# Optimization experiments

Measured on AMD Instinct MI355X. Metric: run time of the kernel, lower is better.

## Reference

```python
import jax, jax.numpy as jnp
import numpy as np

D = 256
H = 16
HD = D // H
N_BIAS = 6
B, E = 8, 1024


def _layernorm(x, g, b, eps=1e-5):
    mu = jnp.mean(x, axis=-1, keepdims=True)
    var = jnp.mean(jnp.square(x - mu), axis=-1, keepdims=True)
    return (x - mu) * jax.lax.rsqrt(var + eps) * g + b


def setup_inputs() -> dict:
    key = jax.random.key(0)
    ks = jax.random.split(key, 16)
    s = 0.02
    inp = {
        "x": jax.random.normal(ks[0], (B, E, D), dtype=jnp.float32),
        "struct_bias": jax.random.randint(ks[1], (B, E, E), 0, N_BIAS),
        "key_padding_mask": jnp.zeros((B, E), dtype=bool),
        # projections stored as [in, out] so y = x @ W + b
        "Wq": jax.random.normal(ks[2], (D, D), jnp.float32) * s,
        "bq": jnp.zeros((D,), jnp.float32),
        "Wk": jax.random.normal(ks[3], (D, D), jnp.float32) * s,
        "bk": jnp.zeros((D,), jnp.float32),
        "Wv": jax.random.normal(ks[4], (D, D), jnp.float32) * s,
        "bv": jnp.zeros((D,), jnp.float32),
        "Wo": jax.random.normal(ks[5], (D, D), jnp.float32) * s,
        "bo": jnp.zeros((D,), jnp.float32),
        "bias_emb": jax.random.normal(ks[6], (N_BIAS, H), jnp.float32) * s,
        "ln1_g": jnp.ones((D,), jnp.float32),
        "ln1_b": jnp.zeros((D,), jnp.float32),
        "W_ff1": jax.random.normal(ks[7], (D, 4 * D), jnp.float32) * s,
        "b_ff1": jnp.zeros((4 * D,), jnp.float32),
        "W_ff2": jax.random.normal(ks[8], (4 * D, D), jnp.float32) * s,
        "b_ff2": jnp.zeros((D,), jnp.float32),
        "ln2_g": jnp.ones((D,), jnp.float32),
        "ln2_b": jnp.zeros((D,), jnp.float32),
    }
    return inp


def reference(x, struct_bias, key_padding_mask, Wq, bq, Wk, bk, Wv, bv, Wo, bo,
              bias_emb, ln1_g, ln1_b, W_ff1, b_ff1, W_ff2, b_ff2, ln2_g, ln2_b):
    b, e, d = x.shape
    # project and split heads: [B, H, E, HD]
    q = (x @ Wq + bq).reshape(b, e, H, HD).transpose(0, 2, 1, 3)
    k = (x @ Wk + bk).reshape(b, e, H, HD).transpose(0, 2, 1, 3)
    v = (x @ Wv + bv).reshape(b, e, H, HD).transpose(0, 2, 1, 3)
    scores = jnp.einsum('bhqd,bhkd->bhqk', q, k) / np.sqrt(HD).astype(np.float32)
    # learned structural bias: [B,E,E,H] -> [B,H,E,E]
    bias = bias_emb[struct_bias].transpose(0, 3, 1, 2)
    scores = scores + bias
    scores = jnp.where(key_padding_mask[:, None, None, :], -jnp.inf, scores)
    attn = jax.nn.softmax(scores, axis=-1)
    out = jnp.einsum('bhqk,bhkd->bhqd', attn, v)
    out = out.transpose(0, 2, 1, 3).reshape(b, e, d)
    out = out @ Wo + bo
    x = _layernorm(x + out, ln1_g, ln1_b)
    ff = jax.nn.gelu(x @ W_ff1 + b_ff1, approximate=False) @ W_ff2 + b_ff2
    x = _layernorm(x + ff, ln2_g, ln2_b)
    return x
```

## Files before the change

kernel.cpp:

```cpp
#include <hip/hip_runtime.h>
#include <math.h>

#define B_  8
#define E_  1024
#define D_  256
#define H_  16
#define FF_ 1024
#define M_  (B_ * E_)

typedef __attribute__((ext_vector_type(8))) short short8;
typedef __attribute__((ext_vector_type(4))) float f32x4;
typedef unsigned short bf16u;

#define GLOAD_LDS16(g, l) __builtin_amdgcn_global_load_lds( \
    (const __attribute__((address_space(1))) void*)(g), \
    (__attribute__((address_space(3))) void*)(l), 16, 0, 0)

__device__ __forceinline__ unsigned short f2bf(float f) {
  union { float f; unsigned u; } c; c.f = f;
  unsigned r = c.u + 0x7fffu + ((c.u >> 16) & 1u);
  return (unsigned short)(r >> 16);
}
__device__ __forceinline__ float gelu_exact(float x) {
  return 0.5f * x * (1.0f + erff(x * 0.70710678118654752f));
}

template<int BM, int BN, int EPI>
__global__ __launch_bounds__(256) void mm_k(
    const bf16u* __restrict__ A, const bf16u* __restrict__ Wt,
    const float* __restrict__ bias, const float* __restrict__ R,
    void* __restrict__ Cout, int M, int N, int K)
{
  constexpr int WM = BM / 2, WN = BN / 2;
  constexpr int MT = WM / 16, NT = WN / 16;
  constexpr int PA = BM * 8 / 256, PB = BN * 8 / 256;
  constexpr int LBM = (BM == 128 ? 7 : 6), LBN = (BN == 128 ? 7 : 6);
  __shared__ bf16u As[BM * 64];
  __shared__ bf16u Bs[BN * 64];

  const int t = threadIdx.x;
  const int l15 = t & 15, quad = (t >> 4) & 3;
  const int w = t >> 6, wm = w >> 1, wn = w & 1;
  const int m0 = blockIdx.x * BM, n0 = blockIdx.y * BN;

  f32x4 acc[MT][NT];
  const f32x4 z4 = {0.f, 0.f, 0.f, 0.f};
#pragma unroll
  for (int i = 0; i < MT; ++i)
#pragma unroll
    for (int j = 0; j < NT; ++j) acc[i][j] = z4;

  for (int k0 = 0; k0 < K; k0 += 64) {
    __syncthreads();
#pragma unroll
    for (int p = 0; p < PA; ++p) {
      int g = p * 256 + t;
      int m = g & (BM - 1), c = g >> LBM;
      const bf16u* src = A + (size_t)(m0 + m) * K + k0 + c * 8;
      GLOAD_LDS16(src, As + g * 8);
    }
#pragma unroll
    for (int p = 0; p < PB; ++p) {
      int g = p * 256 + t;
      int n = g & (BN - 1), c = g >> LBN;
      const bf16u* src = Wt + (size_t)(n0 + n) * K + k0 + c * 8;
      GLOAD_LDS16(src, Bs + g * 8);
    }
    __syncthreads();
#pragma unroll
    for (int s = 0; s < 2; ++s) {
      short8 af[MT], bfr[NT];
#pragma unroll
      for (int mt = 0; mt < MT; ++mt)
        af[mt] = *(const short8*)(As + ((s * 4 + quad) * BM + wm * WM + mt * 16 + l15) * 8);
#pragma unroll
      for (int nt = 0; nt < NT; ++nt)
        bfr[nt] = *(const short8*)(Bs + ((s * 4 + quad) * BN + wn * WN + nt * 16 + l15) * 8);
#pragma unroll
      for (int mt = 0; mt < MT; ++mt)
#pragma unroll
        for (int nt = 0; nt < NT; ++nt)
          acc[mt][nt] = __builtin_amdgcn_mfma_f32_16x16x32_bf16(
              af[mt], bfr[nt], acc[mt][nt], 0, 0, 0);
    }
  }

#pragma unroll
  for (int mt = 0; mt < MT; ++mt) {
#pragma unroll
    for (int nt = 0; nt < NT; ++nt) {
      int col = n0 + wn * WN + nt * 16 + l15;
      float bia = bias[col];
#pragma unroll
      for (int r = 0; r < 4; ++r) {
        int row = m0 + wm * WM + mt * 16 + quad * 4 + r;
        size_t idx = (size_t)row * N + col;
        float v = acc[mt][nt][r] + bia;
        if (EPI == 1)      { ((float*)Cout)[idx] = v + R[idx]; }
        else if (EPI == 2) { ((bf16u*)Cout)[idx] = f2bf(gelu_exact(v)); }
        else               { ((bf16u*)Cout)[idx] = f2bf(v); }
      }
    }
  }
}

__global__ __launch_bounds__(256) void prep_k(
    const float* __restrict__ Wq, const float* __restrict__ Wk,
    const float* __restrict__ Wv, const float* __restrict__ Wo,
    const float* __restrict__ Wf1, const float* __restrict__ Wf2,
    bf16u* __restrict__ Wqkvt, bf16u* __restrict__ Wot,
    bf16u* __restrict__ Wf1t, bf16u* __restrict__ Wf2t,
    const float* __restrict__ bq, const float* __restrict__ bk,
    const float* __restrict__ bv, float* __restrict__ bqkv,
    const float* __restrict__ X, bf16u* __restrict__ Xb)
{
  __shared__ float tile[32][33];
  const int gid = blockIdx.x;
  const int t = threadIdx.x;

  if (gid < 768) {
    const float* src; bf16u* dst; int K, N, bx, by;
    if (gid < 256) {
      const int z = gid >> 6, r = gid & 63;
      src = (z == 0) ? Wq : (z == 1) ? Wk : (z == 2) ? Wv : Wo;
      dst = (z == 0) ? Wqkvt : (z == 1) ? Wqkvt + 65536
          : (z == 2) ? Wqkvt + 131072 : Wot;
      K = 256; N = 256; bx = r & 7; by = r >> 3;
    } else if (gid < 512) {
      const int r = gid - 256;
      src = Wf1; dst = Wf1t; K = 256; N = 1024; bx = r & 7; by = r >> 3;
    } else {
      const int r = gid - 512;
      src = Wf2; dst = Wf2t; K = 1024; N = 256; bx = r & 31; by = r >> 5;
    }
    const int tx = t & 31, ty = t >> 5;
    const int kb = bx * 32, nb = by * 32;
#pragma unroll
    for (int r = 0; r < 4; ++r)
      tile[ty + 8 * r][tx] = src[(size_t)(kb + ty + 8 * r) * N + nb + tx];
    __syncthreads();
#pragma unroll
    for (int r = 0; r < 4; ++r)
      dst[(size_t)(nb + ty + 8 * r) * K + kb + tx] = f2bf(tile[tx][ty + 8 * r]);
  } else if (gid < 771) {
    int i = (gid - 768) * 256 + t;
    bqkv[i] = (i < 256) ? bq[i] : (i < 512) ? bk[i - 256] : bv[i - 512];
  } else {
    int i = (gid - 771) * 256 + t;
    float4 a = ((const float4*)X)[i * 2];
    float4 b = ((const float4*)X)[i * 2 + 1];
    uint4 o;
    o.x = f2bf(a.x) | ((unsigned)f2bf(a.y) << 16);
    o.y = f2bf(a.z) | ((unsigned)f2bf(a.w) << 16);
    o.z = f2bf(b.x) | ((unsigned)f2bf(b.y) << 16);
    o.w = f2bf(b.z) | ((unsigned)f2bf(b.w) << 16);
    ((uint4*)Xb)[i] = o;
  }
}

__global__ __launch_bounds__(256) void attn_k(
    const bf16u* __restrict__ qkv, const int* __restrict__ sb,
    const unsigned char* __restrict__ mask, const float* __restrict__ be,
    bf16u* __restrict__ O)
{
  __shared__ bf16u Kl[2][2][64][40];
  __shared__ bf16u Vt[2][2][2][16][40];
  __shared__ float emb2[6][2];

  const int t    = threadIdx.x;
  const int b    = blockIdx.z;
  const int hg   = blockIdx.y;
  const int w    = t >> 6;
  const int lane = t & 63;
  const int l15  = lane & 15;
  const int quad = lane >> 4;
  const int q0w  = blockIdx.x * 64 + w * 16;
  const float C2 = 0.36067376022224085f;

  if (t < 12) emb2[t >> 1][t & 1] = be[(t >> 1) * 16 + hg * 2 + (t & 1)] * 1.44269504088896f;

  {
    float4 z = {0.f, 0.f, 0.f, 0.f};
    float4* kp = (float4*)&Kl[0][0][0][0];
    for (int i = t; i < 1280; i += 256) kp[i] = z;
  }

  short8 qf[2];
#pragma unroll
  for (int hp = 0; hp < 2; ++hp) {
    uint4 v = {0u, 0u, 0u, 0u};
    if (quad < 2)
      v = *(const uint4*)(qkv + ((size_t)(b * E_) + q0w + l15) * 768 +
                          (hg * 2 + hp) * 16 + quad * 8);
    else if (quad == 2)
      v.x = 0x3F80u;
    union { uint4 u; short8 s; } c; c.u = v;
    qf[hp] = c.s;
  }

  const int s_hp   = t >> 7;
  const int s_key  = (t >> 1) & 63;
  const int s_half = t & 1;
  const int vu     = t & 127;
  const int vz     = vu >> 2;
  const int vh     = (vu >> 1) & 1;
  const int vjh    = vu & 1;
  const int vs2    = vz >> 4;
  const int vrow0  = vh * 8 + vjh * 4;
  const int vc     = ((vz >> 1) & 3) * 8 + ((vz >> 3) & 1) * 4 + (vz & 1) * 2;

  const size_t kvbase = (size_t)b * E_ * 768;
  const bf16u* kbase = qkv + kvbase + 256 + (hg * 2 + s_hp) * 16 + s_half * 8;
  const bf16u* vbase = qkv + kvbase + 512 + (hg * 2 + s_hp) * 16 + vrow0;
  const int* sbp = sb + ((size_t)(b * E_) + q0w + l15) * E_;

  f32x4 accO[2];
  const f32x4 z4 = {0.f, 0.f, 0.f, 0.f};
  accO[0] = z4; accO[1] = z4;
  float lsum[2] = {0.f, 0.f};

  uint4 kA;
  uint2 va, vb;
  unsigned mA;
  int sraw[2][2][4];
  {
    kA = *(const uint4*)(kbase + (size_t)s_key * 768);
    const bf16u* p0 = vbase + (size_t)(2 * vz) * 768;
    va = *(const uint2*)p0;
    vb = *(const uint2*)(p0 + 768);
    mA = mask[b * E_ + s_key];
#pragma unroll
    for (int s2 = 0; s2 < 2; ++s2)
#pragma unroll
      for (int kb2 = 0; kb2 < 2; ++kb2)
        *(int4*)&sraw[s2][kb2][0] =
            *(const int4*)(sbp + s2 * 32 + kb2 * 16 + quad * 4);
  }
  __syncthreads();

#pragma unroll 2
  for (int i = 0; i < 16; ++i) {
    const int cur = i & 1;

    *(uint4*)&Kl[cur][s_hp][s_key][s_half * 8] = kA;
    {
      union { uint2 u; bf16u e[4]; } a, c; a.u = va; c.u = vb;
#pragma unroll
      for (int j = 0; j < 4; ++j)
        *(unsigned*)&Vt[cur][s_hp][vs2][vrow0 + j][vc] =
            (unsigned)a.e[j] | ((unsigned)c.e[j] << 16);
    }
    if (s_half == 0)
      Kl[cur][s_hp][s_key][16] = mA ? (bf16u)0xCF6E : (bf16u)0;

    __syncthreads();

    int srn[2][2][4];
    if (i < 15) {
      const int kn = (i + 1) * 64;
      kA = *(const uint4*)(kbase + (size_t)(kn + s_key) * 768);
      const bf16u* p0 = vbase + (size_t)(kn + 2 * vz) * 768;
      va = *(const uint2*)p0;
      vb = *(const uint2*)(p0 + 768);
      mA = mask[b * E_ + kn + s_key];
#pragma unroll
      for (int s2 = 0; s2 < 2; ++s2)
#pragma unroll
        for (int kb2 = 0; kb2 < 2; ++kb2)
          *(int4*)&srn[s2][kb2][0] =
              *(const int4*)(sbp + kn + s2 * 32 + kb2 * 16 + quad * 4);
    }

#pragma unroll
    for (int s2 = 0; s2 < 2; ++s2) {
      short8 k00 = *(const short8*)&Kl[cur][0][s2 * 32 + l15][quad * 8];
      short8 k01 = *(const short8*)&Kl[cur][0][s2 * 32 + 16 + l15][quad * 8];
      short8 k10 = *(const short8*)&Kl[cur][1][s2 * 32 + l15][quad * 8];
      short8 k11 = *(const short8*)&Kl[cur][1][s2 * 32 + 16 + l15][quad * 8];
      f32x4 sc00 = __builtin_amdgcn_mfma_f32_16x16x32_bf16(k00, qf[0], z4, 0, 0, 0);
      f32x4 sc01 = __builtin_amdgcn_mfma_f32_16x16x32_bf16(k01, qf[0], z4, 0, 0, 0);
      f32x4 sc10 = __builtin_amdgcn_mfma_f32_16x16x32_bf16(k10, qf[1], z4, 0, 0, 0);
      f32x4 sc11 = __builtin_amdgcn_mfma_f32_16x16x32_bf16(k11, qf[1], z4, 0, 0, 0);

      unsigned pk0[4], pk1[4];
#pragma unroll
      for (int r = 0; r < 4; ++r) {
        float2 w0 = *(const float2*)&emb2[sraw[s2][0][r]][0];
        float2 w1 = *(const float2*)&emb2[sraw[s2][1][r]][0];
        float p00 = __builtin_amdgcn_exp2f(fmaf(sc00[r], C2, w0.x));
        float p01 = __builtin_amdgcn_exp2f(fmaf(sc01[r], C2, w1.x));
        float p10 = __builtin_amdgcn_exp2f(fmaf(sc10[r], C2, w0.y));
        float p11 = __builtin_amdgcn_exp2f(fmaf(sc11[r], C2, w1.y));
        unsigned u00 = __float_as_uint(p00), u01 = __float_as_uint(p01);
        unsigned u10 = __float_as_uint(p10), u11 = __float_as_uint(p11);
        lsum[0] += __uint_as_float(u00 & 0xffff0000u) + __uint_as_float(u01 & 0xffff0000u);
        lsum[1] += __uint_as_float(u10 & 0xffff0000u) + __uint_as_float(u11 & 0xffff0000u);
        if ((r & 1) == 0) {
          pk0[r >> 1]       = u00 >> 16;
          pk0[2 + (r >> 1)] = u01 >> 16;
          pk1[r >> 1]       = u10 >> 16;
          pk1[2 + (r >> 1)] = u11 >> 16;
        } else {
          pk0[r >> 1]       |= u00 & 0xffff0000u;
          pk0[2 + (r >> 1)] |= u01 & 0xffff0000u;
          pk1[r >> 1]       |= u10 & 0xffff0000u;
          pk1[2 + (r >> 1)] |= u11 & 0xffff0000u;
        }
      }
      union { unsigned u[4]; short8 s; } a0, a1;
      a0.u[0] = pk0[0]; a0.u[1] = pk0[1]; a0.u[2] = pk0[2]; a0.u[3] = pk0[3];
      a1.u[0] = pk1[0]; a1.u[1] = pk1[1]; a1.u[2] = pk1[2]; a1.u[3] = pk1[3];

      short8 vf0 = *(const short8*)&Vt[cur][0][s2][l15][quad * 8];
      short8 vf1 = *(const short8*)&Vt[cur][1][s2][l15][quad * 8];
      accO[0] = __builtin_amdgcn_mfma_f32_16x16x32_bf16(a0.s, vf0, accO[0], 0, 0, 0);
      accO[1] = __builtin_amdgcn_mfma_f32_16x16x32_bf16(a1.s, vf1, accO[1], 0, 0, 0);
    }

    if (i < 15) {
#pragma unroll
      for (int s2 = 0; s2 < 2; ++s2)
#pragma unroll
        for (int kb2 = 0; kb2 < 2; ++kb2)
#pragma unroll
          for (int r = 0; r < 4; ++r)
            sraw[s2][kb2][r] = srn[s2][kb2][r];
    }
  }

#pragma unroll
  for (int hp = 0; hp < 2; ++hp) {
    lsum[hp] += __shfl_xor(lsum[hp], 16, 64);
    lsum[hp] += __shfl_xor(lsum[hp], 32, 64);
  }
#pragma unroll
  for (int hp = 0; hp < 2; ++hp) {
#pragma unroll
    for (int r = 0; r < 4; ++r) {
      float lq = __shfl(lsum[hp], quad * 4 + r, 64);
      float o = accO[hp][r] / lq;
      O[((size_t)(b * E_) + q0w + quad * 4 + r) * 256 + (hg * 2 + hp) * 16 + l15] = f2bf(o);
    }
  }
}

template<int DUAL>
__global__ __launch_bounds__(256) void ln_k(
    const float* __restrict__ X, const float* __restrict__ g,
    const float* __restrict__ bta, float* __restrict__ Y, bf16u* __restrict__ Yb)
{
  const int row  = blockIdx.x * 4 + (threadIdx.x >> 6);
  const int lane = threadIdx.x & 63;
  float4 v = *(const float4*)(X + (size_t)row * D_ + lane * 4);
  float s  = v.x + v.y + v.z + v.w;
  float ss = v.x * v.x + v.y * v.y + v.z * v.z + v.w * v.w;
#pragma unroll
  for (int off = 32; off; off >>= 1) {
    s  += __shfl_xor(s, off, 64);
    ss += __shfl_xor(ss, off, 64);
  }
  float mu  = s * (1.f / 256.f);
  float var = ss * (1.f / 256.f) - mu * mu;
  float rs  = 1.f / sqrtf(var + 1e-5f);
  float4 gv = *(const float4*)(g + lane * 4);
  float4 bv = *(const float4*)(bta + lane * 4);
  float4 o;
  o.x = (v.x - mu) * rs * gv.x + bv.x;
  o.y = (v.y - mu) * rs * gv.y + bv.y;
  o.z = (v.z - mu) * rs * gv.z + bv.z;
  o.w = (v.w - mu) * rs * gv.w + bv.w;
  *(float4*)(Y + (size_t)row * D_ + lane * 4) = o;
  if (DUAL) {
    uint2 p;
    p.x = f2bf(o.x) | ((unsigned)f2bf(o.y) << 16);
    p.y = f2bf(o.z) | ((unsigned)f2bf(o.w) << 16);
    *(uint2*)(Yb + (size_t)row * D_ + lane * 4) = p;
  }
}

extern "C" void kernel_launch(void* const* d_in, const int* in_sizes, int n_in,
                              void* d_out, int out_size, void* d_ws, size_t ws_size,
                              hipStream_t stream) {
  const float* x   = (const float*)d_in[0];
  const int*   sb  = (const int*)d_in[1];
  const unsigned char* mask = (const unsigned char*)d_in[2];
  const float* Wq  = (const float*)d_in[3];
  const float* bq  = (const float*)d_in[4];
  const float* Wk  = (const float*)d_in[5];
  const float* bk  = (const float*)d_in[6];
  const float* Wv  = (const float*)d_in[7];
  const float* bv  = (const float*)d_in[8];
  const float* Wo  = (const float*)d_in[9];
  const float* bo  = (const float*)d_in[10];
  const float* be  = (const float*)d_in[11];
  const float* g1  = (const float*)d_in[12];
  const float* b1  = (const float*)d_in[13];
  const float* Wf1 = (const float*)d_in[14];
  const float* bf1 = (const float*)d_in[15];
  const float* Wf2 = (const float*)d_in[16];
  const float* bf2 = (const float*)d_in[17];
  const float* g2  = (const float*)d_in[18];
  const float* b2  = (const float*)d_in[19];
  float* out = (float*)d_out;

  char* ws = (char*)d_ws;
  bf16u* Wqkvt = (bf16u*)(ws + 0);
  bf16u* Wot   = (bf16u*)(ws + 393216);
  bf16u* Wf1t  = (bf16u*)(ws + 524288);
  bf16u* Wf2t  = (bf16u*)(ws + 1048576);
  float* bqkv  = (float*)(ws + 1572864);
  bf16u* xb    = (bf16u*)(ws + 2097152);
  bf16u* qkv   = (bf16u*)(ws + 6291456);
  bf16u* att   = (bf16u*)(ws + 18874368);
  float* t1    = (float*)(ws + 23068672);
  float* x1    = (float*)(ws + 31457280);
  bf16u* x1b   = (bf16u*)(ws + 39845888);
  bf16u* ffh   = (bf16u*)(ws + 2097152);
  float* t2    = (float*)(ws + 18874368);

  dim3 blk(256);

  prep_k<<<1795, blk, 0, stream>>>(Wq, Wk, Wv, Wo, Wf1, Wf2,
                                   Wqkvt, Wot, Wf1t, Wf2t,
                                   bq, bk, bv, bqkv, x, xb);

  mm_k<128, 128, 0><<<dim3(64, 6), blk, 0, stream>>>(xb, Wqkvt, bqkv, nullptr,
                                                     qkv, M_, 768, 256);
  attn_k<<<dim3(16, 8, 8), blk, 0, stream>>>(qkv, sb, mask, be, att);

  mm_k<64, 64, 1><<<dim3(128, 4), blk, 0, stream>>>(att, Wot, bo, x,
                                                    t1, M_, 256, 256);
  ln_k<1><<<M_ / 4, blk, 0, stream>>>(t1, g1, b1, x1, x1b);

  mm_k<128, 128, 2><<<dim3(64, 8), blk, 0, stream>>>(x1b, Wf1t, bf1, nullptr,
                                                     ffh, M_, 1024, 256);
  mm_k<64, 64, 1><<<dim3(128, 4), blk, 0, stream>>>(ffh, Wf2t, bf2, x1,
                                                    t2, M_, 256, 1024);
  ln_k<0><<<M_ / 4, blk, 0, stream>>>(t2, g2, b2, out, nullptr);
}
```

Measured before the change: 229.7 us.

## Store QKV head-major, apply key mask in registers, retune output GEMM tiles

The QKV GEMM epilogue now writes Q, K and V in a [batch][head][q/k/v][token][16] layout, so each attention load of K and V reads contiguous 32-byte rows instead of rows with a 768-element stride. The padding mask is no longer folded into the K tile through an extra column and a ones-element in Q. Instead, four mask bytes are loaded per lane and the masked probabilities are zeroed in registers, which lets the K LDS tile shrink from 40 to 16 columns and removes the zero-fill. The softmax/MFMA section is wrapped in s_setprio, and the Wo and FF2 GEMMs switch from 64x64 to 128x64 tiles. The scattered epilogue stores and the smaller grid for the two output GEMMs could reduce store efficiency or occupancy.

```diff
diff --git a/kernel.cpp b/kernel.cpp
--- a/kernel.cpp
+++ b/kernel.cpp
@@ -94,11 +94,17 @@
 #pragma unroll
       for (int r = 0; r < 4; ++r) {
         int row = m0 + wm * WM + mt * 16 + quad * 4 + r;
-        size_t idx = (size_t)row * N + col;
         float v = acc[mt][nt][r] + bia;
-        if (EPI == 1)      { ((float*)Cout)[idx] = v + R[idx]; }
-        else if (EPI == 2) { ((bf16u*)Cout)[idx] = f2bf(gelu_exact(v)); }
-        else               { ((bf16u*)Cout)[idx] = f2bf(v); }
+        if (EPI == 3) {
+          size_t pidx = ((((size_t)(row >> 10) * 16 + ((col >> 4) & 15)) * 3 +
+                          (col >> 8)) * E_ + (row & 1023)) * 16 + (col & 15);
+          ((bf16u*)Cout)[pidx] = f2bf(v);
+        } else {
+          size_t idx = (size_t)row * N + col;
+          if (EPI == 1)      { ((float*)Cout)[idx] = v + R[idx]; }
+          else if (EPI == 2) { ((bf16u*)Cout)[idx] = f2bf(gelu_exact(v)); }
+          else               { ((bf16u*)Cout)[idx] = f2bf(v); }
+        }
       }
     }
   }
@@ -163,7 +169,7 @@
     const unsigned char* __restrict__ mask, const float* __restrict__ be,
     bf16u* __restrict__ O)
 {
-  __shared__ bf16u Kl[2][2][64][40];
+  __shared__ bf16u Kl[2][2][64][16];
   __shared__ bf16u Vt[2][2][2][16][40];
   __shared__ float emb2[6][2];
 
@@ -179,21 +185,13 @@
 
   if (t < 12) emb2[t >> 1][t & 1] = be[(t >> 1) * 16 + hg * 2 + (t & 1)] * 1.44269504088896f;
 
-  {
-    float4 z = {0.f, 0.f, 0.f, 0.f};
-    float4* kp = (float4*)&Kl[0][0][0][0];
-    for (int i = t; i < 1280; i += 256) kp[i] = z;
-  }
-
   short8 qf[2];
 #pragma unroll
   for (int hp = 0; hp < 2; ++hp) {
     uint4 v = {0u, 0u, 0u, 0u};
     if (quad < 2)
-      v = *(const uint4*)(qkv + ((size_t)(b * E_) + q0w + l15) * 768 +
-                          (hg * 2 + hp) * 16 + quad * 8);
-    else if (quad == 2)
-      v.x = 0x3F80u;
+      v = *(const uint4*)(qkv +
+          ((((size_t)b * 16 + hg * 2 + hp) * 3 + 0) * E_ + q0w + l15) * 16 + quad * 8);
     union { uint4 u; short8 s; } c; c.u = v;
     qf[hp] = c.s;
   }
@@ -209,10 +207,10 @@
   const int vrow0  = vh * 8 + vjh * 4;
   const int vc     = ((vz >> 1) & 3) * 8 + ((vz >> 3) & 1) * 4 + (vz & 1) * 2;
 
-  const size_t kvbase = (size_t)b * E_ * 768;
-  const bf16u* kbase = qkv + kvbase + 256 + (hg * 2 + s_hp) * 16 + s_half * 8;
-  const bf16u* vbase = qkv + kvbase + 512 + (hg * 2 + s_hp) * 16 + vrow0;
+  const bf16u* kbase = qkv + (((size_t)b * 16 + hg * 2 + s_hp) * 3 + 1) * E_ * 16 + s_half * 8;
+  const bf16u* vbase = qkv + (((size_t)b * 16 + hg * 2 + s_hp) * 3 + 2) * E_ * 16 + vrow0;
   const int* sbp = sb + ((size_t)(b * E_) + q0w + l15) * E_;
+  const unsigned char* maskp = mask + (size_t)b * E_;
 
   f32x4 accO[2];
   const f32x4 z4 = {0.f, 0.f, 0.f, 0.f};
@@ -221,20 +219,21 @@
 
   uint4 kA;
   uint2 va, vb;
-  unsigned mA;
   int sraw[2][2][4];
+  unsigned mvA[2][2];
   {
-    kA = *(const uint4*)(kbase + (size_t)s_key * 768);
-    const bf16u* p0 = vbase + (size_t)(2 * vz) * 768;
+    kA = *(const uint4*)(kbase + (size_t)s_key * 16);
+    const bf16u* p0 = vbase + (size_t)(2 * vz) * 16;
     va = *(const uint2*)p0;
-    vb = *(const uint2*)(p0 + 768);
-    mA = mask[b * E_ + s_key];
+    vb = *(const uint2*)(p0 + 16);
 #pragma unroll
     for (int s2 = 0; s2 < 2; ++s2)
 #pragma unroll
-      for (int kb2 = 0; kb2 < 2; ++kb2)
+      for (int kb2 = 0; kb2 < 2; ++kb2) {
         *(int4*)&sraw[s2][kb2][0] =
             *(const int4*)(sbp + s2 * 32 + kb2 * 16 + quad * 4);
+        mvA[s2][kb2] = *(const unsigned*)(maskp + s2 * 32 + kb2 * 16 + quad * 4);
+      }
   }
   __syncthreads();
 
@@ -250,37 +249,43 @@
         *(unsigned*)&Vt[cur][s_hp][vs2][vrow0 + j][vc] =
             (unsigned)a.e[j] | ((unsigned)c.e[j] << 16);
     }
-    if (s_half == 0)
-      Kl[cur][s_hp][s_key][16] = mA ? (bf16u)0xCF6E : (bf16u)0;
 
     __syncthreads();
 
     int srn[2][2][4];
+    unsigned mvN[2][2];
     if (i < 15) {
       const int kn = (i + 1) * 64;
-      kA = *(const uint4*)(kbase + (size_t)(kn + s_key) * 768);
-      const bf16u* p0 = vbase + (size_t)(kn + 2 * vz) * 768;
+      kA = *(const uint4*)(kbase + (size_t)(kn + s_key) * 16);
+      const bf16u* p0 = vbase + (size_t)(kn + 2 * vz) * 16;
       va = *(const uint2*)p0;
-      vb = *(const uint2*)(p0 + 768);
-      mA = mask[b * E_ + kn + s_key];
+      vb = *(const uint2*)(p0 + 16);
 #pragma unroll
       for (int s2 = 0; s2 < 2; ++s2)
 #pragma unroll
-        for (int kb2 = 0; kb2 < 2; ++kb2)
+        for (int kb2 = 0; kb2 < 2; ++kb2) {
           *(int4*)&srn[s2][kb2][0] =
               *(const int4*)(sbp + kn + s2 * 32 + kb2 * 16 + quad * 4);
-    }
-
+          mvN[s2][kb2] = *(const unsigned*)(maskp + kn + s2 * 32 + kb2 * 16 + quad * 4);
+        }
+    }
+
+    __builtin_amdgcn_s_setprio(1);
 #pragma unroll
     for (int s2 = 0; s2 < 2; ++s2) {
-      short8 k00 = *(const short8*)&Kl[cur][0][s2 * 32 + l15][quad * 8];
-      short8 k01 = *(const short8*)&Kl[cur][0][s2 * 32 + 16 + l15][quad * 8];
-      short8 k10 = *(const short8*)&Kl[cur][1][s2 * 32 + l15][quad * 8];
-      short8 k11 = *(const short8*)&Kl[cur][1][s2 * 32 + 16 + l15][quad * 8];
-      f32x4 sc00 = __builtin_amdgcn_mfma_f32_16x16x32_bf16(k00, qf[0], z4, 0, 0, 0);
-      f32x4 sc01 = __builtin_amdgcn_mfma_f32_16x16x32_bf16(k01, qf[0], z4, 0, 0, 0);
-      f32x4 sc10 = __builtin_amdgcn_mfma_f32_16x16x32_bf16(k10, qf[1], z4, 0, 0, 0);
-      f32x4 sc11 = __builtin_amdgcn_mfma_f32_16x16x32_bf16(k11, qf[1], z4, 0, 0, 0);
+      union { uint4 u; short8 s; } kc00, kc01, kc10, kc11;
+      kc00.u = (uint4){0u,0u,0u,0u}; kc01.u = (uint4){0u,0u,0u,0u};
+      kc10.u = (uint4){0u,0u,0u,0u}; kc11.u = (uint4){0u,0u,0u,0u};
+      if (quad < 2) {
+        kc00.u = *(const uint4*)&Kl[cur][0][s2 * 32 + l15][quad * 8];
+        kc01.u = *(const uint4*)&Kl[cur][0][s2 * 32 + 16 + l15][quad * 8];
+        kc10.u = *(const uint4*)&Kl[cur][1][s2 * 32 + l15][quad * 8];
+        kc11.u = *(const uint4*)&Kl[cur][1][s2 * 32 + 16 + l15][quad * 8];
+      }
+      f32x4 sc00 = __builtin_amdgcn_mfma_f32_16x16x32_bf16(kc00.s, qf[0], z4, 0, 0, 0);
+      f32x4 sc01 = __builtin_amdgcn_mfma_f32_16x16x32_bf16(kc01.s, qf[0], z4, 0, 0, 0);
+      f32x4 sc10 = __builtin_amdgcn_mfma_f32_16x16x32_bf16(kc10.s, qf[1], z4, 0, 0, 0);
+      f32x4 sc11 = __builtin_amdgcn_mfma_f32_16x16x32_bf16(kc11.s, qf[1], z4, 0, 0, 0);
 
       unsigned pk0[4], pk1[4];
 #pragma unroll
@@ -291,6 +296,10 @@
         float p01 = __builtin_amdgcn_exp2f(fmaf(sc01[r], C2, w1.x));
         float p10 = __builtin_amdgcn_exp2f(fmaf(sc10[r], C2, w0.y));
         float p11 = __builtin_amdgcn_exp2f(fmaf(sc11[r], C2, w1.y));
+        unsigned mb0 = (mvA[s2][0] >> (r * 8)) & 0xffu;
+        unsigned mb1 = (mvA[s2][1] >> (r * 8)) & 0xffu;
+        p00 = mb0 ? 0.f : p00;  p10 = mb0 ? 0.f : p10;
+        p01 = mb1 ? 0.f : p01;  p11 = mb1 ? 0.f : p11;
         unsigned u00 = __float_as_uint(p00), u01 = __float_as_uint(p01);
         unsigned u10 = __float_as_uint(p10), u11 = __float_as_uint(p11);
         lsum[0] += __uint_as_float(u00 & 0xffff0000u) + __uint_as_float(u01 & 0xffff0000u);
@@ -316,15 +325,18 @@
       accO[0] = __builtin_amdgcn_mfma_f32_16x16x32_bf16(a0.s, vf0, accO[0], 0, 0, 0);
       accO[1] = __builtin_amdgcn_mfma_f32_16x16x32_bf16(a1.s, vf1, accO[1], 0, 0, 0);
     }
+    __builtin_amdgcn_s_setprio(0);
 
     if (i < 15) {
 #pragma unroll
       for (int s2 = 0; s2 < 2; ++s2)
 #pragma unroll
-        for (int kb2 = 0; kb2 < 2; ++kb2)
+        for (int kb2 = 0; kb2 < 2; ++kb2) {
 #pragma unroll
           for (int r = 0; r < 4; ++r)
             sraw[s2][kb2][r] = srn[s2][kb2][r];
+          mvA[s2][kb2] = mvN[s2][kb2];
+        }
     }
   }
 
@@ -424,17 +436,17 @@
                                    Wqkvt, Wot, Wf1t, Wf2t,
                                    bq, bk, bv, bqkv, x, xb);
 
-  mm_k<128, 128, 0><<<dim3(64, 6), blk, 0, stream>>>(xb, Wqkvt, bqkv, nullptr,
+  mm_k<128, 128, 3><<<dim3(64, 6), blk, 0, stream>>>(xb, Wqkvt, bqkv, nullptr,
                                                      qkv, M_, 768, 256);
   attn_k<<<dim3(16, 8, 8), blk, 0, stream>>>(qkv, sb, mask, be, att);
 
-  mm_k<64, 64, 1><<<dim3(128, 4), blk, 0, stream>>>(att, Wot, bo, x,
+  mm_k<128, 64, 1><<<dim3(64, 4), blk, 0, stream>>>(att, Wot, bo, x,
                                                     t1, M_, 256, 256);
   ln_k<1><<<M_ / 4, blk, 0, stream>>>(t1, g1, b1, x1, x1b);
 
   mm_k<128, 128, 2><<<dim3(64, 8), blk, 0, stream>>>(x1b, Wf1t, bf1, nullptr,
                                                      ffh, M_, 1024, 256);
-  mm_k<64, 64, 1><<<dim3(128, 4), blk, 0, stream>>>(ffh, Wf2t, bf2, x1,
+  mm_k<128, 64, 1><<<dim3(64, 4), blk, 0, stream>>>(ffh, Wf2t, bf2, x1,
                                                     t2, M_, 256, 1024);
   ln_k<0><<<M_ / 4, blk, 0, stream>>>(t2, g2, b2, out, nullptr);
 }
```

Measured after the change: 239.9 us. 4.4% more time.
